# Kernel tuning notes

Hardware: AMD Instinct MI355X
Metric: run time of the kernel (lower is better)

## Reference

```python
import jax, jax.numpy as jnp
import numpy as np

B, T, F, H, D, L = 64, 1024, 304, 304, 128, 128  # batch, enc len, feat=emb, hidden, dict_size, max_phn_num


def _init(k, sh):
    bound = 1.0 / np.sqrt(H)
    return jax.random.uniform(k, sh, jnp.float32, -bound, bound)


def setup_inputs() -> dict:
    key = jax.random.key(0)
    ks = jax.random.split(key, 12)
    return {
        "x": jax.random.normal(ks[0], (B, T, F), jnp.float32),
        "target": jax.random.randint(ks[1], (B, L, 1), 0, D),
        "emb": jax.random.normal(ks[2], (D, F), jnp.float32),
        "enc_Wih": _init(ks[3], (3 * H, F)),
        "enc_Whh": _init(ks[4], (3 * H, H)),
        "enc_bih": _init(ks[5], (3 * H,)),
        "enc_bhh": _init(ks[6], (3 * H,)),
        "dec_Wih": _init(ks[7], (3 * H, F)),
        "dec_Whh": _init(ks[8], (3 * H, H)),
        "dec_bih": _init(ks[9], (3 * H,)),
        "dec_bhh": _init(ks[10], (3 * H,)),
        "lin_W": _init(ks[11], (D, H)),
        "lin_b": jnp.zeros((D,), jnp.float32),
    }


def gru_step(h, xt, Wih, Whh, bih, bhh):
    # PyTorch GRU cell, gate order (r, z, n)
    gi = xt @ Wih.T + bih            # [B, 3H]
    gh = h @ Whh.T + bhh             # [B, 3H]
    ir, iz, innew = jnp.split(gi, 3, axis=-1)
    hr, hz, hn = jnp.split(gh, 3, axis=-1)
    r = jax.nn.sigmoid(ir + hr)
    z = jax.nn.sigmoid(iz + hz)
    n = jnp.tanh(innew + r * hn)
    return (1.0 - z) * n + z * h


def reference(x, target, emb, enc_Wih, enc_Whh, enc_bih, enc_bhh,
              dec_Wih, dec_Whh, dec_bih, dec_bhh, lin_W, lin_b):
    Bsz = x.shape[0]
    Hdim = enc_Whh.shape[1]
    Lphn = target.shape[1]

    # ---- encoder GRU over acoustic frames ----
    h0 = jnp.zeros((Bsz, Hdim), x.dtype)

    def enc_scan(h, xt):
        return gru_step(h, xt, enc_Wih, enc_Whh, enc_bih, enc_bhh), None

    h_enc, _ = jax.lax.scan(enc_scan, h0, jnp.swapaxes(x, 0, 1))

    tok0 = target[:, 0, 0]  # [B]

    def dec_scan(carry, _):
        h, tok = carry
        e = emb[tok]                                   # [B, F]
        h = gru_step(h, e, dec_Wih, dec_Whh, dec_bih, dec_bhh)
        logits = h @ lin_W.T + lin_b                   # [B, D]
        nxt = jnp.argmax(logits, axis=-1)
        return (h, nxt), logits

    _, logits = jax.lax.scan(dec_scan, (h_enc, tok0), None, length=Lphn)
    softmaxs = jnp.swapaxes(logits, 0, 1)              # [B, L, D]

    softmax_cal = softmaxs[:, :-1, :].reshape(-1, softmaxs.shape[-1])
    target_cal = target[:, 1:, :].reshape(-1)
    asr_outputs = jnp.argmax(softmaxs[:, :-1, :], axis=2)[:, :, None]
    return softmax_cal, target_cal, asr_outputs
```

## Files before the change

### kernel.cpp

```cpp
#include <hip/hip_runtime.h>
#include <cstdint>
#include <cstddef>

#define HN 304
#define G3 912
#define US 76
#define RS 228
#define NB 64
#define TSTEPS 1024
#define LDEC 127
#define DCLS 128

#define OUT_O1 1040384
#define OUT_O2 1048512

static const size_t OFF_GI   = 0;
static const size_t OFF_HP   = 239075328ull;
static const size_t OFF_AM   = 239230976ull;
static const size_t OFF_ABRT = 239233024ull;
static const size_t OFF_TAB  = 239233280ull;
static const size_t WS_NEED  = 239700224ull;

#define SM_LINW   0
#define SM_U      39168
#define SM_HB     40320
#define SM_AMXV   40624
#define SM_AMXI   40628
#define SM_FLOATS 40632
#define SMEM_BYTES (SM_FLOATS * 4)

#define PKFMA_L(C2, A2, B2) \
    asm("v_pk_fma_f32 %0, %1, %2, %0 op_sel:[0,0,0] op_sel_hi:[0,1,1]" \
        : "+v"(C2) : "v"(A2), "v"(B2))
#define PKFMA_H(C2, A2, B2) \
    asm("v_pk_fma_f32 %0, %1, %2, %0 op_sel:[1,0,0] op_sel_hi:[1,1,1]" \
        : "+v"(C2) : "v"(A2), "v"(B2))

#define KEEP4(V) asm volatile("" : "+v"((V).x), "+v"((V).y), "+v"((V).z), "+v"((V).w))

__global__ __launch_bounds__(256) void gi_gemm(const float* __restrict__ X,
                                               const float* __restrict__ W,
                                               const float* __restrict__ bias,
                                               float* __restrict__ out)
{
    __shared__ float As[16][132];
    __shared__ float Bs[16][132];
    const int tid = threadIdx.x;
    const int m0 = blockIdx.x * 128;
    const int n0 = blockIdx.y * 128;
    const int tx = tid & 15;
    const int ty = tid >> 4;
    const int lr = tid >> 1;
    const int lc = (tid & 1) * 8;

    float2 c2[8][4];
#pragma unroll
    for (int i = 0; i < 8; ++i)
#pragma unroll
        for (int j = 0; j < 4; ++j) { c2[i][j].x = 0.f; c2[i][j].y = 0.f; }

    const bool wok = (n0 + lr < G3);
    const float* xrow = X + (size_t)(m0 + lr) * HN;
    const float* wrow = W + (size_t)(n0 + lr) * HN;
    const float4 z4 = make_float4(0.f, 0.f, 0.f, 0.f);

    float4 xa = *(const float4*)(xrow + lc);
    float4 xb = *(const float4*)(xrow + lc + 4);
    float4 wa = wok ? *(const float4*)(wrow + lc) : z4;
    float4 wb = wok ? *(const float4*)(wrow + lc + 4) : z4;

    for (int k0 = 0; k0 < HN; k0 += 16) {
        As[lc + 0][lr] = xa.x; As[lc + 1][lr] = xa.y; As[lc + 2][lr] = xa.z; As[lc + 3][lr] = xa.w;
        As[lc + 4][lr] = xb.x; As[lc + 5][lr] = xb.y; As[lc + 6][lr] = xb.z; As[lc + 7][lr] = xb.w;
        Bs[lc + 0][lr] = wa.x; Bs[lc + 1][lr] = wa.y; Bs[lc + 2][lr] = wa.z; Bs[lc + 3][lr] = wa.w;
        Bs[lc + 4][lr] = wb.x; Bs[lc + 5][lr] = wb.y; Bs[lc + 6][lr] = wb.z; Bs[lc + 7][lr] = wb.w;
        __syncthreads();
        if (k0 + 16 < HN) {
            xa = *(const float4*)(xrow + k0 + 16 + lc);
            xb = *(const float4*)(xrow + k0 + 16 + lc + 4);
            if (wok) {
                wa = *(const float4*)(wrow + k0 + 16 + lc);
                wb = *(const float4*)(wrow + k0 + 16 + lc + 4);
            }
        }
#pragma unroll
        for (int kk = 0; kk < 16; ++kk) {
            const float2* ar = (const float2*)&As[kk][ty * 8];
            const float2* br = (const float2*)&Bs[kk][tx * 8];
            float2 ap[4], bp[4];
#pragma unroll
            for (int j = 0; j < 4; ++j) { ap[j] = ar[j]; bp[j] = br[j]; }
#pragma unroll
            for (int p = 0; p < 4; ++p) {
#pragma unroll
                for (int j = 0; j < 4; ++j) {
                    PKFMA_L(c2[2 * p][j],     ap[p], bp[j]);
                    PKFMA_H(c2[2 * p + 1][j], ap[p], bp[j]);
                }
            }
        }
        __syncthreads();
    }

    const int nb = n0 + tx * 8;
    float4 bb0 = (nb + 3 < G3) ? *(const float4*)(bias + nb) : z4;
    float4 bb1 = (nb + 7 < G3) ? *(const float4*)(bias + nb + 4) : z4;
#pragma unroll
    for (int i = 0; i < 8; ++i) {
        const size_t m = (size_t)(m0 + ty * 8 + i);
        if (nb + 3 < G3) {
            float4 v = make_float4(c2[i][0].x + bb0.x, c2[i][0].y + bb0.y,
                                   c2[i][1].x + bb0.z, c2[i][1].y + bb0.w);
            *(float4*)(out + m * G3 + nb) = v;
        }
        if (nb + 7 < G3) {
            float4 v = make_float4(c2[i][2].x + bb1.x, c2[i][2].y + bb1.y,
                                   c2[i][3].x + bb1.z, c2[i][3].y + bb1.w);
            *(float4*)(out + m * G3 + nb + 4) = v;
        }
    }
}

__global__ __launch_bounds__(256) void table_k(const float* __restrict__ emb,
                                               const float* __restrict__ Wih,
                                               const float* __restrict__ bih,
                                               float* __restrict__ tab)
{
    const int idx = blockIdx.x * 256 + threadIdx.x;
    const int d = idx / G3;
    const int R = idx - d * G3;
    const float4* e4 = (const float4*)(emb + (size_t)d * HN);
    const float4* w4 = (const float4*)(Wih + (size_t)R * HN);
    float acc = 0.f;
#pragma unroll
    for (int j = 0; j < 76; ++j) {
        const float4 e = e4[j], w = w4[j];
        acc += e.x * w.x; acc += e.y * w.y; acc += e.z * w.z; acc += e.w * w.w;
    }
    tab[idx] = acc + bih[R];
}

__global__ void tcal_k(const int* __restrict__ target, float* __restrict__ out)
{
    const int i = blockIdx.x * 256 + threadIdx.x;
    if (i < NB * LDEC) {
        const int b = i / LDEC;
        const int t = i - b * LDEC;
        out[OUT_O1 + i] = (float)target[b * 128 + t + 1];
    }
}

__device__ __forceinline__ void barl()
{
    asm volatile("s_waitcnt lgkmcnt(0)\n\ts_barrier" ::: "memory");
}

__device__ __forceinline__ void pub32(unsigned int* p, unsigned v)
{
    __hip_atomic_store(p, v, __ATOMIC_RELAXED, __HIP_MEMORY_SCOPE_AGENT);
}

__device__ __forceinline__ unsigned poll_tag32(unsigned int* p, unsigned want, int* abortf)
{
    unsigned v; int g = 0;
    for (;;) {
        v = __hip_atomic_load(p, __ATOMIC_RELAXED, __HIP_MEMORY_SCOPE_AGENT);
        if ((v & 3u) == want) break;
        if ((++g & 255) == 0) {
            if (__hip_atomic_load(abortf, __ATOMIC_RELAXED, __HIP_MEMORY_SCOPE_AGENT) != 0) break;
            if (g > (1 << 19)) {
                __hip_atomic_store(abortf, 1, __ATOMIC_RELAXED, __HIP_MEMORY_SCOPE_AGENT);
                break;
            }
        }
    }
    __asm__ volatile("" ::: "memory");
    return v;
}

#define RNN_STEP(T_, GR, GZ, GN) do {                                               \
    if (comp) {                                                                     \
        const float4* hp = (const float4*)(hbuf + ksq * US);                        \
        float acc0 = 0.f, acc1 = 0.f;                                               \
        _Pragma("unroll")                                                           \
        for (int j = 0; j < 19; ++j) {                                              \
            const float4 h4 = hp[j];                                                \
            const float4 w0 = wreg0[j], w1 = wreg1[j];                              \
            acc0 += w0.x * h4.x; acc0 += w0.y * h4.y;                               \
            acc0 += w0.z * h4.z; acc0 += w0.w * h4.w;                               \
            acc1 += w1.x * h4.x; acc1 += w1.y * h4.y;                               \
            acc1 += w1.z * h4.z; acc1 += w1.w * h4.w;                               \
        }                                                                           \
        partU[ksq * RS + lp] = acc0;                                                \
        partU[ksq * RS + lp + 114] = acc1;                                          \
    }                                                                               \
    barl();                                                                         \
    if (tid < US) {                                                                 \
        const float ghr = partU[tid] + partU[RS + tid]                              \
                        + partU[2 * RS + tid] + partU[3 * RS + tid] + b_r;          \
        const float ghz = partU[US + tid] + partU[RS + US + tid]                    \
                        + partU[2 * RS + US + tid] + partU[3 * RS + US + tid] + b_z;\
        const float ghn = partU[2 * US + tid] + partU[RS + 2 * US + tid]            \
                        + partU[2 * RS + 2 * US + tid] + partU[3 * RS + 2 * US + tid] + b_n; \
        const float r_ = 1.f / (1.f + expf(-((GR) + ghr)));                         \
        const float z_ = 1.f / (1.f + expf(-((GZ) + ghz)));                         \
        const float n_ = tanhf((GN) + r_ * ghn);                                    \
        const float hnew = (1.f - z_) * n_ + z_ * hbuf[u];                          \
        const unsigned hb_ = (__float_as_uint(hnew) & ~3u) | ((unsigned)(T_) & 3u); \
        hbuf[u] = __uint_as_float(hb_);                                             \
        pub32(&hpb[((T_) & 1) * NB * HN + u], hb_);                                 \
    }                                                                               \
    if (tid < HN && cq != s) {                                                      \
        const unsigned v_ = poll_tag32(&hpb[((T_) & 1) * NB * HN + tid],            \
                                       (unsigned)(T_) & 3u, abortf);                \
        hbuf[tid] = __uint_as_float(v_);                                            \
    }                                                                               \
    barl();                                                                         \
} while (0)

__global__ __attribute__((amdgpu_waves_per_eu(2, 2)))
__launch_bounds__(512) void rnn_persist(
    const float* __restrict__ gi,
    const float* __restrict__ encWhh, const float* __restrict__ encBhh,
    const float* __restrict__ decWhh, const float* __restrict__ decBhh,
    const float* __restrict__ tab,
    const float* __restrict__ linW, const float* __restrict__ linB,
    const int* __restrict__ target,
    unsigned int* hpk, int* abortf, float* out)
{
    const int w = blockIdx.x;
    const int b = w & 63;
    const int s = w >> 6;
    const int tid = threadIdx.x;

    extern __shared__ float smem[];
    float* linw_s = smem + SM_LINW;
    float* partU  = smem + SM_U;
    float* hbuf   = smem + SM_HB;
    float* amx_vs = smem + SM_AMXV;
    int*   amx_is = (int*)(smem + SM_AMXI);

    const bool comp = (tid < 456);
    const int ksq = tid / 114;
    const int lp  = tid - ksq * 114;
    const int g0 = lp / US,         ul0 = lp - g0 * US;
    const int g1 = (lp + 114) / US, ul1 = (lp + 114) - g1 * US;
    const int Rrow0 = g0 * HN + s * US + ul0;
    const int Rrow1 = g1 * HN + s * US + ul1;
    const int u = s * US + tid;
    const int cq = tid / US;

    unsigned int* hpb = hpk + b * HN;

    for (int i = tid; i < DCLS * HN; i += 512) {
        const int r0 = i / HN;
        linw_s[r0 * 306 + (i - r0 * HN)] = linW[i];
    }
    for (int i = tid; i < HN; i += 512) hbuf[i] = 0.f;

    float4 wreg0[19], wreg1[19];
    if (comp) {
        const float4* wp0 = (const float4*)(encWhh + (size_t)Rrow0 * HN + (size_t)ksq * US);
        const float4* wp1 = (const float4*)(encWhh + (size_t)Rrow1 * HN + (size_t)ksq * US);
#pragma unroll
        for (int j = 0; j < 19; ++j) {
            wreg0[j] = wp0[j]; wreg1[j] = wp1[j];
            KEEP4(wreg0[j]); KEEP4(wreg1[j]);
        }
    }
    float b_r = 0.f, b_z = 0.f, b_n = 0.f;
    if (tid < US) { b_r = encBhh[u]; b_z = encBhh[HN + u]; b_n = encBhh[2 * HN + u]; }

    __syncthreads();

    const float* gib = gi + (size_t)b * TSTEPS * G3;

    float grA = 0.f, gzA = 0.f, gnA = 0.f, grB = 0.f, gzB = 0.f, gnB = 0.f;
    if (tid < US) { grA = gib[u]; gzA = gib[HN + u]; gnA = gib[2 * HN + u]; }

    for (int t = 0; t < TSTEPS; t += 2) {
        if (tid < US) {
            const float* gp = gib + (size_t)(t + 1) * G3;
            grB = gp[u]; gzB = gp[HN + u]; gnB = gp[2 * HN + u];
        }
        RNN_STEP(t + 1, grA, gzA, gnA);
        if (tid < US && t + 2 < TSTEPS) {
            const float* gp = gib + (size_t)(t + 2) * G3;
            grA = gp[u]; gzA = gp[HN + u]; gnA = gp[2 * HN + u];
        }
        RNN_STEP(t + 2, grB, gzB, gnB);
    }

    if (comp) {
        const float4* wp0 = (const float4*)(decWhh + (size_t)Rrow0 * HN + (size_t)ksq * US);
        const float4* wp1 = (const float4*)(decWhh + (size_t)Rrow1 * HN + (size_t)ksq * US);
#pragma unroll
        for (int j = 0; j < 19; ++j) {
            wreg0[j] = wp0[j]; wreg1[j] = wp1[j];
            KEEP4(wreg0[j]); KEEP4(wreg1[j]);
        }
    }
    if (tid < US) { b_r = decBhh[u]; b_z = decBhh[HN + u]; b_n = decBhh[2 * HN + u]; }
    int tok = target[b * 128];
    float linb_r = 0.f;
    if (tid < DCLS) linb_r = linB[tid];
    const int lr128 = tid & 127;
    const int lq = tid >> 7;
    barl();

    for (int t = 0; t < LDEC; ++t) {
        const int T = TSTEPS + 1 + t;
        float gr = 0.f, gz = 0.f, gn = 0.f;
        if (tid < US) {
            const float* tp = tab + (size_t)tok * G3;
            gr = tp[u]; gz = tp[HN + u]; gn = tp[2 * HN + u];
        }
        RNN_STEP(T, gr, gz, gn);

        {
            const float* wl = linw_s + lr128 * 306 + lq * 76;
            const float* hl = hbuf + lq * 76;
            float a0 = 0.f, a1 = 0.f;
#pragma unroll
            for (int j = 0; j < 19; ++j) {
                const float2 wv = *(const float2*)(wl + 2 * j);
                const float2 hv = *(const float2*)(hl + 2 * j);
                a0 += wv.x * hv.x; a0 += wv.y * hv.y;
            }
#pragma unroll
            for (int j = 0; j < 19; ++j) {
                const float2 wv = *(const float2*)(wl + 38 + 2 * j);
                const float2 hv = *(const float2*)(hl + 38 + 2 * j);
                a1 += wv.x * hv.x; a1 += wv.y * hv.y;
            }
            partU[lr128 * 9 + 2 * lq]     = a0;
            partU[lr128 * 9 + 2 * lq + 1] = a1;
        }
        barl();
        if (tid < DCLS) {
            float lg = partU[tid * 9 + 0];
            lg += partU[tid * 9 + 1]; lg += partU[tid * 9 + 2]; lg += partU[tid * 9 + 3];
            lg += partU[tid * 9 + 4]; lg += partU[tid * 9 + 5]; lg += partU[tid * 9 + 6];
            lg += partU[tid * 9 + 7]; lg += linb_r;
            if ((tid >> 5) == s)
                out[((size_t)b * LDEC + t) * DCLS + tid] = lg;
            partU[tid * 9 + 8] = lg;
        }
        barl();
        if (tid < 4) {
            float bv = partU[(tid * 32) * 9 + 8]; int bi = 0;
            for (int i = 1; i < 32; ++i) {
                const float v = partU[(tid * 32 + i) * 9 + 8];
                if (v > bv) { bv = v; bi = i; }
            }
            amx_vs[tid] = bv; amx_is[tid] = tid * 32 + bi;
        }
        barl();
        {
            float gbv = amx_vs[0]; int gbi = amx_is[0];
            if (amx_vs[1] > gbv) { gbv = amx_vs[1]; gbi = amx_is[1]; }
            if (amx_vs[2] > gbv) { gbv = amx_vs[2]; gbi = amx_is[2]; }
            if (amx_vs[3] > gbv) { gbv = amx_vs[3]; gbi = amx_is[3]; }
            tok = gbi;
            if (tid == 0 && s == 0) out[OUT_O2 + (size_t)b * LDEC + t] = (float)gbi;
        }
    }
}

extern "C" void kernel_launch(void* const* d_in, const int* in_sizes, int n_in,
                              void* d_out, int out_size, void* d_ws, size_t ws_size,
                              hipStream_t stream)
{
    (void)in_sizes; (void)n_in; (void)out_size;
    const float* x      = (const float*)d_in[0];
    const int*   target = (const int*)  d_in[1];
    const float* emb    = (const float*)d_in[2];
    const float* encWih = (const float*)d_in[3];
    const float* encWhh = (const float*)d_in[4];
    const float* encBih = (const float*)d_in[5];
    const float* encBhh = (const float*)d_in[6];
    const float* decWih = (const float*)d_in[7];
    const float* decWhh = (const float*)d_in[8];
    const float* decBih = (const float*)d_in[9];
    const float* decBhh = (const float*)d_in[10];
    const float* linW   = (const float*)d_in[11];
    const float* linB   = (const float*)d_in[12];
    float* out = (float*)d_out;
    char* ws = (char*)d_ws;

    if (ws_size < WS_NEED) return;

    float*        gi   = (float*)(ws + OFF_GI);
    unsigned int* hpk  = (unsigned int*)(ws + OFF_HP);
    int*          abrt = (int*)(ws + OFF_ABRT);
    float*        tab  = (float*)(ws + OFF_TAB);

    static bool s_attr_done = false;
    if (!s_attr_done) {
        (void)hipFuncSetAttribute(reinterpret_cast<const void*>(rnn_persist),
                                  hipFuncAttributeMaxDynamicSharedMemorySize, SMEM_BYTES);
        s_attr_done = true;
    }

    (void)hipMemsetAsync(ws + OFF_HP, 0, OFF_TAB - OFF_HP, stream);
    gi_gemm<<<dim3(512, 8), 256, 0, stream>>>(x, encWih, encBih, gi);
    table_k<<<456, 256, 0, stream>>>(emb, decWih, decBih, tab);
    tcal_k<<<32, 256, 0, stream>>>(target, out);
    rnn_persist<<<256, 512, SMEM_BYTES, stream>>>(gi, encWhh, encBhh, decWhh, decBhh, tab,
                                                  linW, linB, target, hpk, abrt, out);
}
```

Baseline: 3.158 ms.

## Process two batch rows per persistent block with 8-way hidden-unit split

Each persistent workgroup now handles two batch elements and a 38-unit slice across eight blocks, instead of one batch element and a 76-unit slice across four blocks. Every Whh register row is reused for both hidden states, which halves per-thread weight registers and doubles the useful FMAs per weight load. Cross-block hidden-state exchange uses a dual-address polling routine. The decoder logits are restructured as pair-reductions via shuffles computing both batch rows. The cost is more cross-block synchronisation partners per step (eight slices) and more polled values per block.

```diff
diff --git a/kernel.cpp b/kernel.cpp
--- a/kernel.cpp
+++ b/kernel.cpp
@@ -4,8 +4,8 @@
 
 #define HN 304
 #define G3 912
-#define US 76
-#define RS 228
+#define UW 38
+#define KQ 76
 #define NB 64
 #define TSTEPS 1024
 #define LDEC 127
@@ -22,11 +22,11 @@
 static const size_t WS_NEED  = 239700224ull;
 
 #define SM_LINW   0
-#define SM_U      39168
-#define SM_HB     40320
-#define SM_AMXV   40624
-#define SM_AMXI   40628
-#define SM_FLOATS 40632
+#define SM_HB     39168
+#define SM_U      39776
+#define SM_AMXV   40688
+#define SM_AMXI   40696
+#define SM_FLOATS 40704
 #define SMEM_BYTES (SM_FLOATS * 4)
 
 #define PKFMA_L(C2, A2, B2) \
@@ -37,6 +37,8 @@
         : "+v"(C2) : "v"(A2), "v"(B2))
 
 #define KEEP4(V) asm volatile("" : "+v"((V).x), "+v"((V).y), "+v"((V).z), "+v"((V).w))
+
+#define REP19(M) M(0) M(1) M(2) M(3) M(4) M(5) M(6) M(7) M(8) M(9) M(10) M(11) M(12) M(13) M(14) M(15) M(16) M(17) M(18)
 
 __global__ __launch_bounds__(256) void gi_gemm(const float* __restrict__ X,
                                                const float* __restrict__ W,
@@ -178,42 +180,85 @@
     return v;
 }
 
+__device__ __forceinline__ void poll2(unsigned int* pa, unsigned int* pb, unsigned want,
+                                      int* abortf, unsigned& va, unsigned& vb)
+{
+    int g = 0; bool da = false, db = false;
+    for (;;) {
+        if (!da) { unsigned v = __hip_atomic_load(pa, __ATOMIC_RELAXED, __HIP_MEMORY_SCOPE_AGENT);
+                   if ((v & 3u) == want) { va = v; da = true; } }
+        if (!db) { unsigned v = __hip_atomic_load(pb, __ATOMIC_RELAXED, __HIP_MEMORY_SCOPE_AGENT);
+                   if ((v & 3u) == want) { vb = v; db = true; } }
+        if (da && db) break;
+        if ((++g & 255) == 0) {
+            if (__hip_atomic_load(abortf, __ATOMIC_RELAXED, __HIP_MEMORY_SCOPE_AGENT) != 0) break;
+            if (g > (1 << 19)) {
+                __hip_atomic_store(abortf, 1, __ATOMIC_RELAXED, __HIP_MEMORY_SCOPE_AGENT);
+                break;
+            }
+        }
+    }
+    __asm__ volatile("" ::: "memory");
+}
+
+#define DECLW(j) float4 w##j;
+#define LDWJ(j)  w##j = wp_[j]; KEEP4(w##j);
+#define LOAD_WEIGHTS(SRC) do { if (comp) { \
+    const float4* wp_ = (const float4*)((SRC) + (size_t)Rrow * HN + (size_t)ksq * KQ); \
+    REP19(LDWJ) } } while (0)
+
+#define MACJ(j) { const float4 h0v = hp0[j], h1v = hp1[j]; \
+    a0 += w##j.x * h0v.x; a0 += w##j.y * h0v.y; a0 += w##j.z * h0v.z; a0 += w##j.w * h0v.w; \
+    a1 += w##j.x * h1v.x; a1 += w##j.y * h1v.y; a1 += w##j.z * h1v.z; a1 += w##j.w * h1v.w; }
+
 #define RNN_STEP(T_, GR, GZ, GN) do {                                               \
     if (comp) {                                                                     \
-        const float4* hp = (const float4*)(hbuf + ksq * US);                        \
-        float acc0 = 0.f, acc1 = 0.f;                                               \
-        _Pragma("unroll")                                                           \
-        for (int j = 0; j < 19; ++j) {                                              \
-            const float4 h4 = hp[j];                                                \
-            const float4 w0 = wreg0[j], w1 = wreg1[j];                              \
-            acc0 += w0.x * h4.x; acc0 += w0.y * h4.y;                               \
-            acc0 += w0.z * h4.z; acc0 += w0.w * h4.w;                               \
-            acc1 += w1.x * h4.x; acc1 += w1.y * h4.y;                               \
-            acc1 += w1.z * h4.z; acc1 += w1.w * h4.w;                               \
-        }                                                                           \
-        partU[ksq * RS + lp] = acc0;                                                \
-        partU[ksq * RS + lp + 114] = acc1;                                          \
+        const float4* hp0 = (const float4*)(hbq + ksq * KQ);                        \
+        const float4* hp1 = (const float4*)(hbq + 304 + ksq * KQ);                  \
+        float a0 = 0.f, a1 = 0.f;                                                   \
+        REP19(MACJ)                                                                 \
+        partU[ksq * 114 + rr] = a0;                                                 \
+        partU[456 + ksq * 114 + rr] = a1;                                           \
     }                                                                               \
     barl();                                                                         \
-    if (tid < US) {                                                                 \
-        const float ghr = partU[tid] + partU[RS + tid]                              \
-                        + partU[2 * RS + tid] + partU[3 * RS + tid] + b_r;          \
-        const float ghz = partU[US + tid] + partU[RS + US + tid]                    \
-                        + partU[2 * RS + US + tid] + partU[3 * RS + US + tid] + b_z;\
-        const float ghn = partU[2 * US + tid] + partU[RS + 2 * US + tid]            \
-                        + partU[2 * RS + 2 * US + tid] + partU[3 * RS + 2 * US + tid] + b_n; \
+    if (tid < 76) {                                                                 \
+        const int pb_ = fq * 456;                                                   \
+        const float ghr = partU[pb_ + fu] + partU[pb_ + 114 + fu]                   \
+                        + partU[pb_ + 228 + fu] + partU[pb_ + 342 + fu] + b_r;      \
+        const float ghz = partU[pb_ + UW + fu] + partU[pb_ + 114 + UW + fu]         \
+                        + partU[pb_ + 228 + UW + fu] + partU[pb_ + 342 + UW + fu] + b_z; \
+        const float ghn = partU[pb_ + 2 * UW + fu] + partU[pb_ + 114 + 2 * UW + fu] \
+                        + partU[pb_ + 228 + 2 * UW + fu] + partU[pb_ + 342 + 2 * UW + fu] + b_n; \
         const float r_ = 1.f / (1.f + expf(-((GR) + ghr)));                         \
         const float z_ = 1.f / (1.f + expf(-((GZ) + ghz)));                         \
         const float n_ = tanhf((GN) + r_ * ghn);                                    \
-        const float hnew = (1.f - z_) * n_ + z_ * hbuf[u];                          \
+        const float hnew = (1.f - z_) * n_ + z_ * hbq[fq * 304 + un];               \
         const unsigned hb_ = (__float_as_uint(hnew) & ~3u) | ((unsigned)(T_) & 3u); \
-        hbuf[u] = __uint_as_float(hb_);                                             \
-        pub32(&hpb[((T_) & 1) * NB * HN + u], hb_);                                 \
+        hbq[fq * 304 + un] = __uint_as_float(hb_);                                  \
+        pub32(hpk + (size_t)(b0 + fq) * HN + ((T_) & 1) * (NB * HN) + un, hb_);     \
     }                                                                               \
-    if (tid < HN && cq != s) {                                                      \
-        const unsigned v_ = poll_tag32(&hpb[((T_) & 1) * NB * HN + tid],            \
-                                       (unsigned)(T_) & 3u, abortf);                \
-        hbuf[tid] = __uint_as_float(v_);                                            \
+    {                                                                               \
+        const int pq_ = (tid >= 304) ? 1 : 0;                                       \
+        const int pu_ = tid - 304 * pq_;                                            \
+        const bool needA = (pu_ / UW != s);                                         \
+        const int su_ = 208 + tid;                                                  \
+        const bool needB = (tid < 96) && (su_ / UW != s);                           \
+        unsigned va_, vb_;                                                          \
+        if (needA && needB) {                                                       \
+            poll2(hpk + (size_t)(b0 + pq_) * HN + ((T_) & 1) * (NB * HN) + pu_,     \
+                  hpk + (size_t)b1 * HN + ((T_) & 1) * (NB * HN) + su_,             \
+                  (unsigned)(T_) & 3u, abortf, va_, vb_);                           \
+            hbq[pq_ * 304 + pu_] = __uint_as_float(va_);                            \
+            hbq[304 + su_] = __uint_as_float(vb_);                                  \
+        } else if (needA) {                                                         \
+            va_ = poll_tag32(hpk + (size_t)(b0 + pq_) * HN + ((T_) & 1) * (NB * HN) + pu_, \
+                             (unsigned)(T_) & 3u, abortf);                          \
+            hbq[pq_ * 304 + pu_] = __uint_as_float(va_);                            \
+        } else if (needB) {                                                         \
+            vb_ = poll_tag32(hpk + (size_t)b1 * HN + ((T_) & 1) * (NB * HN) + su_,  \
+                             (unsigned)(T_) & 3u, abortf);                          \
+            hbq[304 + su_] = __uint_as_float(vb_);                                  \
+        }                                                                           \
     }                                                                               \
     barl();                                                                         \
 } while (0)
@@ -229,131 +274,130 @@
     unsigned int* hpk, int* abortf, float* out)
 {
     const int w = blockIdx.x;
-    const int b = w & 63;
-    const int s = w >> 6;
+    const int p = w & 31;
+    const int s = w >> 5;
+    const int b0 = 2 * p, b1 = 2 * p + 1;
     const int tid = threadIdx.x;
 
     extern __shared__ float smem[];
     float* linw_s = smem + SM_LINW;
+    float* hbq    = smem + SM_HB;
     float* partU  = smem + SM_U;
-    float* hbuf   = smem + SM_HB;
     float* amx_vs = smem + SM_AMXV;
     int*   amx_is = (int*)(smem + SM_AMXI);
 
     const bool comp = (tid < 456);
     const int ksq = tid / 114;
-    const int lp  = tid - ksq * 114;
-    const int g0 = lp / US,         ul0 = lp - g0 * US;
-    const int g1 = (lp + 114) / US, ul1 = (lp + 114) - g1 * US;
-    const int Rrow0 = g0 * HN + s * US + ul0;
-    const int Rrow1 = g1 * HN + s * US + ul1;
-    const int u = s * US + tid;
-    const int cq = tid / US;
-
-    unsigned int* hpb = hpk + b * HN;
+    const int rr  = tid - ksq * 114;
+    const int gg  = rr / UW;
+    const int ulr = rr - gg * UW;
+    const int Rrow = gg * HN + s * UW + ulr;
+
+    const int fq = (tid < 76) ? (tid / UW) : 0;
+    const int fu = tid - (tid / UW) * UW;
+    const int un = s * UW + ((tid < 76) ? fu : 0);
 
     for (int i = tid; i < DCLS * HN; i += 512) {
         const int r0 = i / HN;
         linw_s[r0 * 306 + (i - r0 * HN)] = linW[i];
     }
-    for (int i = tid; i < HN; i += 512) hbuf[i] = 0.f;
-
-    float4 wreg0[19], wreg1[19];
-    if (comp) {
-        const float4* wp0 = (const float4*)(encWhh + (size_t)Rrow0 * HN + (size_t)ksq * US);
-        const float4* wp1 = (const float4*)(encWhh + (size_t)Rrow1 * HN + (size_t)ksq * US);
-#pragma unroll
-        for (int j = 0; j < 19; ++j) {
-            wreg0[j] = wp0[j]; wreg1[j] = wp1[j];
-            KEEP4(wreg0[j]); KEEP4(wreg1[j]);
-        }
-    }
+    for (int i = tid; i < 608; i += 512) hbq[i] = 0.f;
+
+    REP19(DECLW)
+    LOAD_WEIGHTS(encWhh);
     float b_r = 0.f, b_z = 0.f, b_n = 0.f;
-    if (tid < US) { b_r = encBhh[u]; b_z = encBhh[HN + u]; b_n = encBhh[2 * HN + u]; }
+    if (tid < 76) { b_r = encBhh[un]; b_z = encBhh[HN + un]; b_n = encBhh[2 * HN + un]; }
 
     __syncthreads();
 
-    const float* gib = gi + (size_t)b * TSTEPS * G3;
-
-    float grA = 0.f, gzA = 0.f, gnA = 0.f, grB = 0.f, gzB = 0.f, gnB = 0.f;
-    if (tid < US) { grA = gib[u]; gzA = gib[HN + u]; gnA = gib[2 * HN + u]; }
+    const float* gib = gi + (size_t)(b0 + fq) * TSTEPS * G3;
+
+    float gAr = 0.f, gAz = 0.f, gAn = 0.f, gBr = 0.f, gBz = 0.f, gBn = 0.f;
+    if (tid < 76) { gAr = gib[un]; gAz = gib[HN + un]; gAn = gib[2 * HN + un]; }
 
     for (int t = 0; t < TSTEPS; t += 2) {
-        if (tid < US) {
+        if (tid < 76) {
             const float* gp = gib + (size_t)(t + 1) * G3;
-            grB = gp[u]; gzB = gp[HN + u]; gnB = gp[2 * HN + u];
-        }
-        RNN_STEP(t + 1, grA, gzA, gnA);
-        if (tid < US && t + 2 < TSTEPS) {
+            gBr = gp[un]; gBz = gp[HN + un]; gBn = gp[2 * HN + un];
+        }
+        RNN_STEP(t + 1, gAr, gAz, gAn);
+        if (tid < 76 && t + 2 < TSTEPS) {
             const float* gp = gib + (size_t)(t + 2) * G3;
-            grA = gp[u]; gzA = gp[HN + u]; gnA = gp[2 * HN + u];
-        }
-        RNN_STEP(t + 2, grB, gzB, gnB);
-    }
-
-    if (comp) {
-        const float4* wp0 = (const float4*)(decWhh + (size_t)Rrow0 * HN + (size_t)ksq * US);
-        const float4* wp1 = (const float4*)(decWhh + (size_t)Rrow1 * HN + (size_t)ksq * US);
-#pragma unroll
-        for (int j = 0; j < 19; ++j) {
-            wreg0[j] = wp0[j]; wreg1[j] = wp1[j];
-            KEEP4(wreg0[j]); KEEP4(wreg1[j]);
-        }
-    }
-    if (tid < US) { b_r = decBhh[u]; b_z = decBhh[HN + u]; b_n = decBhh[2 * HN + u]; }
-    int tok = target[b * 128];
-    float linb_r = 0.f;
-    if (tid < DCLS) linb_r = linB[tid];
-    const int lr128 = tid & 127;
-    const int lq = tid >> 7;
+            gAr = gp[un]; gAz = gp[HN + un]; gAn = gp[2 * HN + un];
+        }
+        RNN_STEP(t + 2, gBr, gBz, gBn);
+    }
+
+    LOAD_WEIGHTS(decWhh);
+    if (tid < 76) { b_r = decBhh[un]; b_z = decBhh[HN + un]; b_n = decBhh[2 * HN + un]; }
+    int tok0 = target[b0 * 128];
+    int tok1 = target[b1 * 128];
+    const int rp   = tid >> 1;
+    const int lrow = rp & 127;
+    const int lq   = rp >> 7;
+    const int kh   = tid & 1;
+    const float linb_r = linB[lrow];
     barl();
 
     for (int t = 0; t < LDEC; ++t) {
         const int T = TSTEPS + 1 + t;
         float gr = 0.f, gz = 0.f, gn = 0.f;
-        if (tid < US) {
-            const float* tp = tab + (size_t)tok * G3;
-            gr = tp[u]; gz = tp[HN + u]; gn = tp[2 * HN + u];
+        if (tid < 76) {
+            const float* tp = tab + (size_t)(fq ? tok1 : tok0) * G3;
+            gr = tp[un]; gz = tp[HN + un]; gn = tp[2 * HN + un];
         }
         RNN_STEP(T, gr, gz, gn);
 
         {
-            const float* wl = linw_s + lr128 * 306 + lq * 76;
-            const float* hl = hbuf + lq * 76;
-            float a0 = 0.f, a1 = 0.f;
+            const float* wl = linw_s + lrow * 306 + kh * 152;
+            const float* hl = hbq + lq * 304 + kh * 152;
+            float p0 = 0.f, p1 = 0.f, p2 = 0.f, p3 = 0.f;
 #pragma unroll
             for (int j = 0; j < 19; ++j) {
                 const float2 wv = *(const float2*)(wl + 2 * j);
                 const float2 hv = *(const float2*)(hl + 2 * j);
-                a0 += wv.x * hv.x; a0 += wv.y * hv.y;
+                p0 += wv.x * hv.x; p0 += wv.y * hv.y;
             }
 #pragma unroll
             for (int j = 0; j < 19; ++j) {
                 const float2 wv = *(const float2*)(wl + 38 + 2 * j);
                 const float2 hv = *(const float2*)(hl + 38 + 2 * j);
-                a1 += wv.x * hv.x; a1 += wv.y * hv.y;
-            }
-            partU[lr128 * 9 + 2 * lq]     = a0;
-            partU[lr128 * 9 + 2 * lq + 1] = a1;
+                p1 += wv.x * hv.x; p1 += wv.y * hv.y;
+            }
+#pragma unroll
+            for (int j = 0; j < 19; ++j) {
+                const float2 wv = *(const float2*)(wl + 76 + 2 * j);
+                const float2 hv = *(const float2*)(hl + 76 + 2 * j);
+                p2 += wv.x * hv.x; p2 += wv.y * hv.y;
+            }
+#pragma unroll
+            for (int j = 0; j < 19; ++j) {
+                const float2 wv = *(const float2*)(wl + 114 + 2 * j);
+                const float2 hv = *(const float2*)(hl + 114 + 2 * j);
+                p3 += wv.x * hv.x; p3 += wv.y * hv.y;
+            }
+            const float q0 = __shfl_xor(p0, 1);
+            const float q1 = __shfl_xor(p1, 1);
+            const float q2 = __shfl_xor(p2, 1);
+            const float q3 = __shfl_xor(p3, 1);
+            if (!(tid & 1)) {
+                float lg = p0; lg += p1; lg += p2; lg += p3;
+                lg += q0; lg += q1; lg += q2; lg += q3; lg += linb_r;
+                partU[rp] = lg;
+                if ((lrow >> 4) == s)
+                    out[((size_t)(b0 + lq) * LDEC + t) * DCLS + lrow] = lg;
+            }
         }
         barl();
-        if (tid < DCLS) {
-            float lg = partU[tid * 9 + 0];
-            lg += partU[tid * 9 + 1]; lg += partU[tid * 9 + 2]; lg += partU[tid * 9 + 3];
-            lg += partU[tid * 9 + 4]; lg += partU[tid * 9 + 5]; lg += partU[tid * 9 + 6];
-            lg += partU[tid * 9 + 7]; lg += linb_r;
-            if ((tid >> 5) == s)
-                out[((size_t)b * LDEC + t) * DCLS + tid] = lg;
-            partU[tid * 9 + 8] = lg;
-        }
-        barl();
-        if (tid < 4) {
-            float bv = partU[(tid * 32) * 9 + 8]; int bi = 0;
+        if (tid < 8) {
+            const int q_ = tid >> 2, grp = tid & 3;
+            const float* lp_ = partU + q_ * 128 + grp * 32;
+            float bv = lp_[0]; int bi = 0;
             for (int i = 1; i < 32; ++i) {
-                const float v = partU[(tid * 32 + i) * 9 + 8];
+                const float v = lp_[i];
                 if (v > bv) { bv = v; bi = i; }
             }
-            amx_vs[tid] = bv; amx_is[tid] = tid * 32 + bi;
+            amx_vs[tid] = bv; amx_is[tid] = grp * 32 + bi;
         }
         barl();
         {
@@ -361,8 +405,16 @@
             if (amx_vs[1] > gbv) { gbv = amx_vs[1]; gbi = amx_is[1]; }
             if (amx_vs[2] > gbv) { gbv = amx_vs[2]; gbi = amx_is[2]; }
             if (amx_vs[3] > gbv) { gbv = amx_vs[3]; gbi = amx_is[3]; }
-            tok = gbi;
-            if (tid == 0 && s == 0) out[OUT_O2 + (size_t)b * LDEC + t] = (float)gbi;
+            tok0 = gbi;
+            float gbv1 = amx_vs[4]; int gbi1 = amx_is[4];
+            if (amx_vs[5] > gbv1) { gbv1 = amx_vs[5]; gbi1 = amx_is[5]; }
+            if (amx_vs[6] > gbv1) { gbv1 = amx_vs[6]; gbi1 = amx_is[6]; }
+            if (amx_vs[7] > gbv1) { gbv1 = amx_vs[7]; gbi1 = amx_is[7]; }
+            tok1 = gbi1;
+            if (tid == 0 && s == 0) {
+                out[OUT_O2 + (size_t)b0 * LDEC + t] = (float)tok0;
+                out[OUT_O2 + (size_t)b1 * LDEC + t] = (float)tok1;
+            }
         }
     }
 }
```

New measurement: 4.938 ms. +56.4%, slower.
